# Kernel tuning notes

Measured on AMD Instinct MI355X. Metric: run time of the kernel, lower is better.

Reference implementation:

```python
import jax, jax.numpy as jnp
import numpy as np

TAU = 2.0  # self.temperature
EPS = 1e-7


def setup_inputs() -> dict:
    key = jax.random.key(0)
    kx, km, kw, kb, kc, kg = jax.random.split(key, 6)
    B, S, H = 8, 2048, 512
    G, V, D = 2, 320, 256  # num_groups, num_vars, codevector_dim
    hidden_states = jax.random.normal(kx, (B, S, H), dtype=jnp.float32)
    mask_time_indices = jax.random.randint(km, (B, S), 0, 2) > 0
    # nn.Linear(H, G*V)
    lim = 1.0 / np.sqrt(H)
    W_proj = jax.random.uniform(kw, (H, G * V), minval=-lim, maxval=lim, dtype=jnp.float32)
    b_proj = jax.random.uniform(kb, (G * V,), minval=-lim, maxval=lim, dtype=jnp.float32)
    codevectors = jax.random.normal(kc, (1, G * V, D // G), dtype=jnp.float32)
    # precomputed gumbel noise for determinism (torch samples inside gumbel_softmax)
    gumbels = jax.random.gumbel(kg, (B * S * G, V), dtype=jnp.float32)
    return {
        "hidden_states": hidden_states,
        "mask_time_indices": mask_time_indices,
        "W_proj": W_proj,
        "b_proj": b_proj,
        "codevectors": codevectors,
        "gumbels": gumbels,
    }


def reference(hidden_states, mask_time_indices, W_proj, b_proj, codevectors, gumbels):
    B, S, H = hidden_states.shape
    GV = W_proj.shape[1]
    V = gumbels.shape[-1]
    G = GV // V
    N = B * S

    logits = hidden_states @ W_proj + b_proj              # [B,S,G*V]
    flat = logits.reshape(N * G, V).astype(jnp.float32)    # [N*G, V]

    # gumbel_softmax(tau=TAU, hard=True) with straight-through estimator
    y_soft = jax.nn.softmax((flat + gumbels) / TAU, axis=-1)
    y_hard = jax.nn.one_hot(jnp.argmax(y_soft, axis=-1), V, dtype=y_soft.dtype)
    probs = y_hard + y_soft - jax.lax.stop_gradient(y_soft)  # [N*G, V]

    # perplexity from the (non-gumbel) soft distribution, masked marginals
    soft_dist = jax.nn.softmax(flat.reshape(N, G, V), axis=-1)
    m = mask_time_indices.reshape(-1).astype(soft_dist.dtype)  # [N]
    marginal = jnp.einsum('ngv,n->gv', soft_dist, m) / jnp.sum(m)
    perplexity = jnp.exp(-jnp.sum(marginal * jnp.log(marginal + EPS), axis=-1)).sum()

    # codebook combine: grouped one-hot mixture (avoids [N, G*V, D/G] blowup)
    cb = codevectors.reshape(G, V, -1)                     # [G, V, D/G]
    codevecs = jnp.einsum('ngv,gvd->ngd', probs.reshape(N, G, V), cb)
    codevecs = codevecs.reshape(B, S, -1)                  # [B, S, D]
    return codevecs, perplexity
```

## Files before the change

kernel.cpp:

```cpp
#include <hip/hip_runtime.h>
#include <hip/hip_bf16.h>
#include <math.h>

constexpr int Mn = 16384;
constexpr int Kd = 512;
constexpr int GV = 640;
constexpr int Vn = 320;
constexpr int Gn = 2;
constexpr int DG = 128;
constexpr float EPSc = 1e-7f;

constexpr int K2 = 1536;
constexpr int KA = 1024;
constexpr int NT = K2 / 32;

typedef _Float16 half8 __attribute__((ext_vector_type(8)));
typedef _Float16 half4 __attribute__((ext_vector_type(4)));
typedef float floatx4 __attribute__((ext_vector_type(4)));

__global__ __launch_bounds__(256) void convert_all(const float* __restrict__ h,
                                                   const float* __restrict__ W,
                                                   _Float16* __restrict__ A2,
                                                   _Float16* __restrict__ B2T,
                                                   float* __restrict__ marg) {
  const int bid = blockIdx.x;
  if (bid < 2048) {
    const int total = Mn * Kd / 4;
    for (int idx = bid * 256 + threadIdx.x; idx < total; idx += 2048 * 256) {
      float4 x = reinterpret_cast<const float4*>(h)[idx];
      int m = idx >> 7;
      int c = (idx & 127) << 2;
      half4 h0, h1;
      float xs[4] = {x.x, x.y, x.z, x.w};
#pragma unroll
      for (int j = 0; j < 4; ++j) {
        _Float16 a = (_Float16)xs[j];
        h0[j] = a;
        h1[j] = (_Float16)(xs[j] - (float)a);
      }
      *reinterpret_cast<half4*>(&A2[(size_t)m * KA + c]) = h0;
      *reinterpret_cast<half4*>(&A2[(size_t)m * KA + Kd + c]) = h1;
    }
  } else if (bid < 2208) {
    const int b2 = bid - 2048;
    const int wave = threadIdx.x >> 6, lane = threadIdx.x & 63;
    const int n = b2 * 4 + wave;
    _Float16* row = B2T + (size_t)n * K2;
#pragma unroll
    for (int j = 0; j < 8; ++j) {
      const int k = lane + 64 * j;
      const float w = W[(size_t)k * GV + n];
      const _Float16 w0 = (_Float16)w;
      const _Float16 w1 = (_Float16)(w - (float)w0);
      row[k] = w0;
      row[Kd + k] = w0;
      row[2 * Kd + k] = w1;
    }
  } else {
    for (int i = threadIdx.x; i <= GV; i += 256) marg[i] = 0.f;
  }
}

__global__ __launch_bounds__(256) void gemm_f16x2(const _Float16* __restrict__ A2,
                                                  const _Float16* __restrict__ B2T,
                                                  const float* __restrict__ bias,
                                                  float* __restrict__ C) {
  __shared__ _Float16 As[2][128 * 32];
  __shared__ _Float16 Bs[2][128 * 32];

  const int bid = blockIdx.x;
  const int sw = (bid & 7) * 80 + (bid >> 3);
  const int mt = sw / 5, nt = sw % 5;
  const int m0 = mt * 128, n0 = nt * 128;

  const int t = threadIdx.x, wv = t >> 6, l = t & 63;
  const int wr = wv >> 1, wc = wv & 1;
  const int lr = l & 15, lk = l >> 4;

  floatx4 acc[4][4] = {};

  auto stage = [&](int buf, int kt) {
    const int k2 = kt * 32;
    const int kA = k2 >= KA ? k2 - KA : k2;
#pragma unroll
    for (int i = 0; i < 2; ++i) {
      const int idx = i * 256 + t;
      const int r = idx >> 2, s2 = idx & 3;
      const int sp = s2 ^ ((r >> 1) & 3);
      const _Float16* ga = A2 + (size_t)(m0 + r) * KA + kA + sp * 8;
      _Float16* la = &As[buf][(i * 256 + wv * 64) * 8];
      __builtin_amdgcn_global_load_lds((const __attribute__((address_space(1))) void*)ga,
                                       (__attribute__((address_space(3))) void*)la, 16, 0, 0);
    }
#pragma unroll
    for (int i = 0; i < 2; ++i) {
      const int idx = i * 256 + t;
      const int r = idx >> 2, s2 = idx & 3;
      const int sp = s2 ^ ((r >> 1) & 3);
      const _Float16* gb = B2T + (size_t)(n0 + r) * K2 + k2 + sp * 8;
      _Float16* lb = &Bs[buf][(i * 256 + wv * 64) * 8];
      __builtin_amdgcn_global_load_lds((const __attribute__((address_space(1))) void*)gb,
                                       (__attribute__((address_space(3))) void*)lb, 16, 0, 0);
    }
  };

  stage(0, 0);
  __syncthreads();
  int cur = 0;
  for (int kt = 0; kt < NT; ++kt) {
    if (kt + 1 < NT) stage(cur ^ 1, kt + 1);

    half8 af[4], bf[4];
#pragma unroll
    for (int mi = 0; mi < 4; ++mi) {
      const int row = wr * 64 + mi * 16 + lr;
      const int sp = lk ^ ((row >> 1) & 3);
      af[mi] = *reinterpret_cast<const half8*>(&As[cur][row * 32 + sp * 8]);
    }
#pragma unroll
    for (int ni = 0; ni < 4; ++ni) {
      const int row = wc * 64 + ni * 16 + lr;
      const int sp = lk ^ ((row >> 1) & 3);
      bf[ni] = *reinterpret_cast<const half8*>(&Bs[cur][row * 32 + sp * 8]);
    }
#pragma unroll
    for (int mi = 0; mi < 4; ++mi)
#pragma unroll
      for (int ni = 0; ni < 4; ++ni)
        acc[mi][ni] = __builtin_amdgcn_mfma_f32_16x16x32_f16(af[mi], bf[ni], acc[mi][ni], 0, 0, 0);

    __syncthreads();
    cur ^= 1;
  }

#pragma unroll
  for (int ni = 0; ni < 4; ++ni) {
    const int gcol = n0 + wc * 64 + ni * 16 + lr;
    const float bv = bias[gcol];
#pragma unroll
    for (int mi = 0; mi < 4; ++mi) {
      const int grow = m0 + wr * 64 + mi * 16 + lk * 4;
#pragma unroll
      for (int j = 0; j < 4; ++j)
        C[(size_t)(grow + j) * GV + gcol] = acc[mi][ni][j] + bv;
    }
  }
}

__global__ __launch_bounds__(256) void row_kernel(const float* __restrict__ logits,
                                                  const float* __restrict__ gumbels,
                                                  const int* __restrict__ mask,
                                                  const float* __restrict__ codevectors,
                                                  float* __restrict__ out,
                                                  float* __restrict__ part,
                                                  float* __restrict__ marg) {
  __shared__ float lmarg[GV];
  const int wave = threadIdx.x >> 6, lane = threadIdx.x & 63;
  const int g = wave & 1;
  const int stream = wave >> 1;
  const int nbase = blockIdx.x * 8 + stream * 4;

  if (threadIdx.x < 8) {
    const int mk = (mask[blockIdx.x * 8 + threadIdx.x] != 0) ? 1 : 0;
    const unsigned long long b = __ballot(mk);
    if (threadIdx.x == 0) atomicAdd(&marg[GV], (float)__popcll(b & 0xFFull));
  }

  float acc[5] = {0.f, 0.f, 0.f, 0.f, 0.f};

  for (int it = 0; it < 2; ++it) {
    const int na = nbase + it * 2, nb = na + 1;
    const float* lrA = logits + (size_t)na * GV + g * Vn;
    const float* grA = gumbels + ((size_t)na * Gn + g) * Vn;
    const float* lrB = logits + (size_t)nb * GV + g * Vn;
    const float* grB = gumbels + ((size_t)nb * Gn + g) * Vn;

    float4 lA = reinterpret_cast<const float4*>(lrA)[lane];
    float4 gA = reinterpret_cast<const float4*>(grA)[lane];
    float lsA = lrA[256 + lane], gsA = grA[256 + lane];
    float4 lB = reinterpret_cast<const float4*>(lrB)[lane];
    float4 gB = reinterpret_cast<const float4*>(grB)[lane];
    float lsB = lrB[256 + lane], gsB = grB[256 + lane];

    float vA[5] = {lA.x, lA.y, lA.z, lA.w, lsA};
    float yA[5] = {lA.x + gA.x, lA.y + gA.y, lA.z + gA.z, lA.w + gA.w, lsA + gsA};
    float vB[5] = {lB.x, lB.y, lB.z, lB.w, lsB};
    float yB[5] = {lB.x + gB.x, lB.y + gB.y, lB.z + gB.z, lB.w + gB.w, lsB + gsB};

    float amA = yA[0], amB = yB[0];
    int aiA = lane * 4, aiB = lane * 4;
#pragma unroll
    for (int j = 1; j < 5; ++j) {
      const int v = (j < 4) ? lane * 4 + j : 256 + lane;
      if (yA[j] > amA) { amA = yA[j]; aiA = v; }
      if (yB[j] > amB) { amB = yB[j]; aiB = v; }
    }
#pragma unroll
    for (int off = 32; off; off >>= 1) {
      const float oA = __shfl_xor(amA, off);
      const int iA = __shfl_xor(aiA, off);
      if (oA > amA || (oA == amA && iA < aiA)) { amA = oA; aiA = iA; }
      const float oB = __shfl_xor(amB, off);
      const int iB = __shfl_xor(aiB, off);
      if (oB > amB || (oB == amB && iB < aiB)) { amB = oB; aiB = iB; }
    }

    float eA[5], eB[5], sA = 0.f, sB = 0.f;
#pragma unroll
    for (int j = 0; j < 5; ++j) {
      eA[j] = expf(vA[j]); sA += eA[j];
      eB[j] = expf(vB[j]); sB += eB[j];
    }
#pragma unroll
    for (int off = 32; off; off >>= 1) {
      sA += __shfl_xor(sA, off);
      sB += __shfl_xor(sB, off);
    }
    const float invA = 1.0f / sA, invB = 1.0f / sB;

    if (mask[na] != 0) {
#pragma unroll
      for (int j = 0; j < 5; ++j) acc[j] += eA[j] * invA;
    }
    if (mask[nb] != 0) {
#pragma unroll
      for (int j = 0; j < 5; ++j) acc[j] += eB[j] * invB;
    }

    const float* cvA = codevectors + ((size_t)g * Vn + aiA) * DG;
    float* orA = out + (size_t)na * (Gn * DG) + g * DG;
    orA[lane] = cvA[lane];
    orA[lane + 64] = cvA[lane + 64];
    const float* cvB = codevectors + ((size_t)g * Vn + aiB) * DG;
    float* orB = out + (size_t)nb * (Gn * DG) + g * DG;
    orB[lane] = cvB[lane];
    orB[lane + 64] = cvB[lane + 64];
  }

  if (stream == 0) {
#pragma unroll
    for (int j = 0; j < 4; ++j) lmarg[g * Vn + lane * 4 + j] = acc[j];
    lmarg[g * Vn + 256 + lane] = acc[4];
  }
  __syncthreads();
  if (stream == 1) {
#pragma unroll
    for (int j = 0; j < 4; ++j) lmarg[g * Vn + lane * 4 + j] += acc[j];
    lmarg[g * Vn + 256 + lane] += acc[4];
  }
  __syncthreads();
  float* prow = part + (size_t)blockIdx.x * GV;
  for (int i = threadIdx.x; i < GV; i += 256) prow[i] = lmarg[i];
}

__global__ __launch_bounds__(64) void reduce_marg(const float* __restrict__ part,
                                                  float* __restrict__ marg) {
  const int c = blockIdx.x * 64 + threadIdx.x;
  const int r0 = blockIdx.y * 64;
  float s = 0.f;
#pragma unroll 8
  for (int r = 0; r < 64; ++r) s += part[(size_t)(r0 + r) * GV + c];
  atomicAdd(&marg[c], s);
}

__global__ __launch_bounds__(640) void finalize(const float* __restrict__ marg,
                                                float* __restrict__ out_pp) {
  __shared__ float wred[10];
  const int t = threadIdx.x, wave = t >> 6, lane = t & 63;
  const float msum = marg[GV];

  const float p = marg[t] / msum;
  float e = p * logf(p + EPSc);
#pragma unroll
  for (int off = 32; off; off >>= 1) e += __shfl_xor(e, off);
  if (lane == 0) wred[wave] = e;
  __syncthreads();
  if (t == 0) {
    const float e0 = wred[0] + wred[1] + wred[2] + wred[3] + wred[4];
    const float e1 = wred[5] + wred[6] + wred[7] + wred[8] + wred[9];
    out_pp[0] = expf(-e0) + expf(-e1);
  }
}

extern "C" void kernel_launch(void* const* d_in, const int* in_sizes, int n_in,
                              void* d_out, int out_size, void* d_ws, size_t ws_size,
                              hipStream_t stream) {
  const float* hidden      = (const float*)d_in[0];
  const int*   mask        = (const int*)d_in[1];
  const float* W           = (const float*)d_in[2];
  const float* bias        = (const float*)d_in[3];
  const float* codevectors = (const float*)d_in[4];
  const float* gumbels     = (const float*)d_in[5];
  float* out = (float*)d_out;

  const size_t cBytes  = (size_t)Mn * GV * sizeof(float);
  const size_t a2Off   = cBytes + 8192;
  const size_t a2Bytes = (size_t)Mn * KA * sizeof(_Float16);
  const size_t b2tOff  = a2Off + a2Bytes;

  float*    logits = (float*)d_ws;
  float*    marg   = (float*)((char*)d_ws + cBytes);
  _Float16* A2     = (_Float16*)((char*)d_ws + a2Off);
  _Float16* B2T    = (_Float16*)((char*)d_ws + b2tOff);
  float*    part   = (float*)A2;

  convert_all<<<2209, 256, 0, stream>>>(hidden, W, A2, B2T, marg);
  gemm_f16x2<<<640, 256, 0, stream>>>(A2, B2T, bias, logits);
  row_kernel<<<Mn / 8, 256, 0, stream>>>(logits, gumbels, mask, codevectors, out, part, marg);
  reduce_marg<<<dim3(10, 32), 64, 0, stream>>>(part, marg);
  finalize<<<1, 640, 0, stream>>>(marg, out + (size_t)Mn * (Gn * DG));
}
```

Before: 115.5 us.

## Triple-buffer GEMM LDS staging with explicit vmcnt waits and single barrier

```diff
diff --git a/kernel.cpp b/kernel.cpp
--- a/kernel.cpp
+++ b/kernel.cpp
@@ -17,6 +17,8 @@
 typedef _Float16 half8 __attribute__((ext_vector_type(8)));
 typedef _Float16 half4 __attribute__((ext_vector_type(4)));
 typedef float floatx4 __attribute__((ext_vector_type(4)));
+
+#define WAITV(N) asm volatile("s_waitcnt vmcnt(" #N ")" ::: "memory")
 
 __global__ __launch_bounds__(256) void convert_all(const float* __restrict__ h,
                                                    const float* __restrict__ W,
@@ -65,8 +67,8 @@
                                                   const _Float16* __restrict__ B2T,
                                                   const float* __restrict__ bias,
                                                   float* __restrict__ C) {
-  __shared__ _Float16 As[2][128 * 32];
-  __shared__ _Float16 Bs[2][128 * 32];
+  __shared__ _Float16 As[3 * 128 * 32];
+  __shared__ _Float16 Bs[3 * 128 * 32];
 
   const int bid = blockIdx.x;
   const int sw = (bid & 7) * 80 + (bid >> 3);
@@ -82,13 +84,15 @@
   auto stage = [&](int buf, int kt) {
     const int k2 = kt * 32;
     const int kA = k2 >= KA ? k2 - KA : k2;
+    _Float16* abase = &As[buf * 4096];
+    _Float16* bbase = &Bs[buf * 4096];
 #pragma unroll
     for (int i = 0; i < 2; ++i) {
       const int idx = i * 256 + t;
       const int r = idx >> 2, s2 = idx & 3;
       const int sp = s2 ^ ((r >> 1) & 3);
       const _Float16* ga = A2 + (size_t)(m0 + r) * KA + kA + sp * 8;
-      _Float16* la = &As[buf][(i * 256 + wv * 64) * 8];
+      _Float16* la = abase + (i * 256 + wv * 64) * 8;
       __builtin_amdgcn_global_load_lds((const __attribute__((address_space(1))) void*)ga,
                                        (__attribute__((address_space(3))) void*)la, 16, 0, 0);
     }
@@ -98,39 +102,49 @@
       const int r = idx >> 2, s2 = idx & 3;
       const int sp = s2 ^ ((r >> 1) & 3);
       const _Float16* gb = B2T + (size_t)(n0 + r) * K2 + k2 + sp * 8;
-      _Float16* lb = &Bs[buf][(i * 256 + wv * 64) * 8];
+      _Float16* lb = bbase + (i * 256 + wv * 64) * 8;
       __builtin_amdgcn_global_load_lds((const __attribute__((address_space(1))) void*)gb,
                                        (__attribute__((address_space(3))) void*)lb, 16, 0, 0);
     }
   };
 
   stage(0, 0);
-  __syncthreads();
-  int cur = 0;
+  stage(1, 1);
+
+  int rb = 0, sb = 2;
   for (int kt = 0; kt < NT; ++kt) {
-    if (kt + 1 < NT) stage(cur ^ 1, kt + 1);
-
+    if (kt < NT - 1) { WAITV(4); } else { WAITV(0); }
+    __builtin_amdgcn_s_barrier();
+    __builtin_amdgcn_sched_barrier(0);
+
+    const _Float16* abase = &As[rb * 4096];
+    const _Float16* bbase = &Bs[rb * 4096];
     half8 af[4], bf[4];
 #pragma unroll
     for (int mi = 0; mi < 4; ++mi) {
       const int row = wr * 64 + mi * 16 + lr;
       const int sp = lk ^ ((row >> 1) & 3);
-      af[mi] = *reinterpret_cast<const half8*>(&As[cur][row * 32 + sp * 8]);
+      af[mi] = *reinterpret_cast<const half8*>(&abase[row * 32 + sp * 8]);
     }
 #pragma unroll
     for (int ni = 0; ni < 4; ++ni) {
       const int row = wc * 64 + ni * 16 + lr;
       const int sp = lk ^ ((row >> 1) & 3);
-      bf[ni] = *reinterpret_cast<const half8*>(&Bs[cur][row * 32 + sp * 8]);
-    }
+      bf[ni] = *reinterpret_cast<const half8*>(&bbase[row * 32 + sp * 8]);
+    }
+
+    if (kt + 2 < NT) stage(sb, kt + 2);
+
+    __builtin_amdgcn_s_setprio(1);
 #pragma unroll
     for (int mi = 0; mi < 4; ++mi)
 #pragma unroll
       for (int ni = 0; ni < 4; ++ni)
         acc[mi][ni] = __builtin_amdgcn_mfma_f32_16x16x32_f16(af[mi], bf[ni], acc[mi][ni], 0, 0, 0);
-
-    __syncthreads();
-    cur ^= 1;
+    __builtin_amdgcn_s_setprio(0);
+
+    rb = (rb == 2) ? 0 : rb + 1;
+    sb = (sb == 2) ? 0 : sb + 1;
   }
 
 #pragma unroll
```

Measured after the change: 108.6 us (median of 2 runs). 1.06x faster.
